# Kernel optimization log

Measured on AMD Instinct MI355X. Metric: run time of the kernel, lower is better.

The kernel has to match this reference:

```python
import jax, jax.numpy as jnp
import numpy as np

N_TOKENS = 16384
D_MODEL = 1024
N_SEG = 4
H_SEG = 1024  # intermediate_size (4096) // num_segments


def setup_inputs() -> dict:
    key = jax.random.key(0)
    kx, ki, kg, ku, kd = jax.random.split(key, 5)
    x = jax.random.normal(kx, (N_TOKENS, D_MODEL), dtype=jnp.float32)
    token_segment_indices = jax.random.randint(ki, (N_TOKENS,), 0, N_SEG, dtype=jnp.int64)
    s = 1.0 / np.sqrt(D_MODEL)
    # weights stored [seg, in, out] for x @ W
    gate_w = jax.random.normal(kg, (N_SEG, D_MODEL, H_SEG), dtype=jnp.float32) * s
    up_w = jax.random.normal(ku, (N_SEG, D_MODEL, H_SEG), dtype=jnp.float32) * s
    down_w = jax.random.normal(kd, (N_SEG, H_SEG, D_MODEL), dtype=jnp.float32) * (1.0 / np.sqrt(H_SEG))
    return {
        'x': x,
        'gate_w': gate_w,
        'up_w': up_w,
        'down_w': down_w,
        'token_segment_indices': token_segment_indices,
    }


def reference(x, gate_w, up_w, down_w, token_segment_indices):
    # _forward_with_indices: each token is processed only by its assigned
    # segment's SwiGLU FFN; all other contributions are zero.  We compute each
    # segment densely and mask (jit-friendly, same math as gather->ffn->scatter).
    out = jnp.zeros_like(x)
    for s in range(N_SEG):
        hidden = jax.nn.silu(x @ gate_w[s]) * (x @ up_w[s])  # [N, H_SEG]
        y = hidden @ down_w[s]                                # [N, D_MODEL]
        mask = (token_segment_indices == s)[:, None]
        out = out + jnp.where(mask, y, 0.0)
    return out
```

## Files before the change

### kernel.cpp

```cpp
#include <hip/hip_runtime.h>
#include <hip/hip_bf16.h>
#include <math.h>

#define NT   16384
#define DM   1024
#define NSEG 4
#define BK   64
#define HS   1024

typedef __attribute__((ext_vector_type(8))) short bf16x8;
typedef __attribute__((ext_vector_type(4))) float f32x4;

typedef __attribute__((address_space(1))) unsigned int gu32;
typedef __attribute__((address_space(3))) unsigned int lu32;

__device__ __forceinline__ void gll16(const void* g, void* l) {
  __builtin_amdgcn_global_load_lds((gu32*)(unsigned long long)g,
                                   (lu32*)(unsigned int)(unsigned long long)l,
                                   16, 0, 0);
}

__device__ __forceinline__ unsigned short cvt_bf16(float f) {
  unsigned int u = __float_as_uint(f);
  u += 0x7fffu + ((u >> 16) & 1u);
  return (unsigned short)(u >> 16);
}


__global__ __launch_bounds__(256) void k_prepw(
    const int* __restrict__ idx, int* __restrict__ part,
    const float* __restrict__ gw, const float* __restrict__ uw, const float* __restrict__ dw,
    unsigned short* __restrict__ gwt, unsigned short* __restrict__ uwt,
    unsigned short* __restrict__ dwt) {
  __shared__ float tile[64][65];
  const int bid = blockIdx.x, tid = threadIdx.x;
  if (bid < 64) {
    __shared__ int sc[5];
    if (tid < 5) sc[tid] = 0;
    __syncthreads();
    int lane = tid & 63;
    int w32 = idx[bid * 256 + tid];
    unsigned long long m = __ballot((tid & 1) && (w32 != 0));
    if (lane == 0 && m) atomicAdd(&sc[4], 1);
    __syncthreads();
    int is32 = (sc[4] != 0);
    int s = w32;
    if (!is32) s = idx[bid * 512 + 2 * tid];
#pragma unroll
    for (int q = 0; q < 4; ++q) {
      m = __ballot(s == q);
      if (lane == 0 && m) atomicAdd(&sc[q], (int)__popcll(m));
    }
    __syncthreads();
    if (tid < 4) part[bid * 8 + tid] = sc[tid];
    if (tid == 4) part[bid * 8 + 4] = is32;
    return;
  }
  int tb = bid - 64;
  int mtx = tb >> 10, seg = (tb >> 8) & 3, tl = tb & 255;
  const float* src = (mtx == 0 ? gw : mtx == 1 ? uw : dw) + (size_t)seg * DM * HS;
  unsigned short* dst = (mtx == 0 ? gwt : mtx == 1 ? uwt : dwt) + (size_t)seg * DM * HS;
  int n0 = (tl & 15) * 64, k0 = (tl >> 4) * 64;
  int col = tid & 63, rb = tid >> 6;
#pragma unroll
  for (int i = 0; i < 64; i += 4)
    tile[i + rb][col] = src[(size_t)(k0 + i + rb) * 1024 + n0 + col];
  __syncthreads();
  int kp = tid & 31, nb = tid >> 5;
#pragma unroll
  for (int j = 0; j < 64; j += 8) {
    int nn = j + nb;
    unsigned int w = (unsigned)cvt_bf16(tile[2 * kp][nn]) |
                     ((unsigned)cvt_bf16(tile[2 * kp + 1][nn]) << 16);
    *(unsigned int*)(dst + (size_t)(n0 + nn) * 1024 + k0 + 2 * kp) = w;
  }
}

__global__ __launch_bounds__(256) void k_cvtrank(
    const int* __restrict__ idx, const int* __restrict__ part,
    const float4* __restrict__ x,
    int* __restrict__ meta, int2* __restrict__ table,
    int* __restrict__ perm, uint4* __restrict__ xc) {
  __shared__ int cnt[64][4];
  __shared__ int wsum[4][4];
  __shared__ int tot[4], pref[4], gbase[4];
  __shared__ int rnk8[8];
  __shared__ int flag_s;
  const int tid = threadIdx.x, bid = blockIdx.x;
  const int lane = tid & 63, wv = tid >> 6;
  const int c = bid >> 5;
  const int p0 = (bid & 31) * 8;

  if (tid == 0) flag_s = part[c * 8 + 4];
  if (wv == 0) {
#pragma unroll
    for (int s = 0; s < 4; ++s) cnt[lane][s] = part[lane * 8 + s];
  }
  __syncthreads();
  const int is32 = flag_s;
  int tok = c * 256 + tid;
  int s_t = is32 ? idx[tok] : idx[2 * tok];
  int myr = 0;
  unsigned long long lt = (1ull << lane) - 1;
#pragma unroll
  for (int q = 0; q < 4; ++q) {
    unsigned long long m = __ballot(s_t == q);
    if (lane == 0) wsum[wv][q] = (int)__popcll(m);
    if (s_t == q) myr = (int)__popcll(m & lt);
  }
  __syncthreads();
  if (tid < 4) {
    int s = tid, t = 0, p = 0;
    for (int b = 0; b < 64; ++b) { if (b == c) p = t; t += cnt[b][s]; }
    tot[s] = t; pref[s] = p;
  }
  __syncthreads();
  if (tid == 0) {
    gbase[0] = 0;
    for (int s = 1; s < 4; ++s) gbase[s] = gbase[s - 1] + tot[s - 1];
    if (bid == 0) {
      int nt = 0;
      for (int s = 0; s < 4; ++s) {
        meta[s] = tot[s]; meta[5 + s] = gbase[s];
        for (int m0 = 0; m0 < tot[s]; m0 += 128) table[nt++] = make_int2(s, m0);
      }
      for (; nt < 132; ++nt) table[nt] = make_int2(-1, 0);
    }
  }
  __syncthreads();
  int wpre = 0;
  for (int w2 = 0; w2 < wv; ++w2) wpre += wsum[w2][s_t];
  int r = gbase[s_t] + pref[s_t] + wpre + myr;
  if (tid >= p0 && tid < p0 + 8) {
    perm[r] = tok;
    rnk8[tid - p0] = r;
  }
  __syncthreads();
  const int j = tid >> 5, l2 = tid & 31;
  const int tok8 = bid * 8 + j;
  const float4* src = x + (size_t)tok8 * 256;
  uint4* dst = xc + (size_t)rnk8[j] * 128;
#pragma unroll
  for (int it = 0; it < 4; ++it) {
    float4 a = src[it * 64 + l2 * 2];
    float4 b = src[it * 64 + l2 * 2 + 1];
    uint4 o;
    o.x = cvt_bf16(a.x) | ((unsigned)cvt_bf16(a.y) << 16);
    o.y = cvt_bf16(a.z) | ((unsigned)cvt_bf16(a.w) << 16);
    o.z = cvt_bf16(b.x) | ((unsigned)cvt_bf16(b.y) << 16);
    o.w = cvt_bf16(b.z) | ((unsigned)cvt_bf16(b.w) << 16);
    dst[it * 32 + l2] = o;
  }
}

__global__ __launch_bounds__(256) void k_gateup(
    const unsigned short* __restrict__ xc,
    const unsigned short* __restrict__ gwt,
    const unsigned short* __restrict__ uwt,
    const int* __restrict__ meta,
    const int2* __restrict__ table,
    unsigned short* __restrict__ hidden) {
  __shared__ __align__(16) unsigned short As[128 * BK];
  __shared__ __align__(16) unsigned short Bg[64 * BK];
  __shared__ __align__(16) unsigned short Bu[64 * BK];
  const int bid = blockIdx.x, tid = threadIdx.x;
  const int2 te = table[bid >> 4];
  if (te.x < 0) return;
  const int seg = te.x, m0 = te.y;
  const int count = meta[seg], base = meta[5 + seg];
  const int n0 = (bid & 15) * 64;

  const int lane = tid & 63;
  const int wave = tid >> 6;

  const unsigned short* ap[4];
#pragma unroll
  for (int is = 0; is < 4; ++is) {
    int c = is * 256 + tid;
    int m = c >> 3;
    int kb = (c & 7) ^ (m & 7);
    int row = m0 + m;
    row = row < count ? row : count - 1;
    ap[is] = xc + (size_t)(base + row) * DM + kb * 8;
  }
  const unsigned short *gp[2], *up[2];
#pragma unroll
  for (int is = 0; is < 2; ++is) {
    int c = is * 256 + tid;
    int n = c >> 3;
    int kb = (c & 7) ^ (n & 7);
    gp[is] = gwt + (size_t)(seg * HS + n0 + n) * DM + kb * 8;
    up[is] = uwt + (size_t)(seg * HS + n0 + n) * DM + kb * 8;
  }

  f32x4 accg[4][2] = {};
  f32x4 accu[4][2] = {};
  const int wm = (wave & 1) * 64;
  const int wn = (wave >> 1) * 32;
  const int fm = lane & 15;
  const int fq = lane >> 4;
  const int fx = lane & 7;
  const int a_e0 = (wm + fm) * 64 + ((fq) ^ fx) * 8;
  const int a_e1 = (wm + fm) * 64 + ((4 + fq) ^ fx) * 8;
  const int b_e0 = (wn + fm) * 64 + ((fq) ^ fx) * 8;
  const int b_e1 = (wn + fm) * 64 + ((4 + fq) ^ fx) * 8;

  for (int kt = 0; kt < DM / BK; ++kt) {
    __syncthreads();
#pragma unroll
    for (int is = 0; is < 4; ++is)
      gll16(ap[is], (char*)As + (is * 256 + wave * 64) * 16);
#pragma unroll
    for (int is = 0; is < 2; ++is) {
      gll16(gp[is], (char*)Bg + (is * 256 + wave * 64) * 16);
      gll16(up[is], (char*)Bu + (is * 256 + wave * 64) * 16);
    }
#pragma unroll
    for (int is = 0; is < 4; ++is) ap[is] += BK;
#pragma unroll
    for (int is = 0; is < 2; ++is) { gp[is] += BK; up[is] += BK; }
    __syncthreads();
#pragma unroll
    for (int s = 0; s < 2; ++s) {
      const unsigned short* Ap = As + (s ? a_e1 : a_e0);
      const unsigned short* Gp = Bg + (s ? b_e1 : b_e0);
      const unsigned short* Up = Bu + (s ? b_e1 : b_e0);
      bf16x8 af[4], bg2[2], bu2[2];
#pragma unroll
      for (int mi = 0; mi < 4; ++mi) af[mi] = *(const bf16x8*)(Ap + mi * 1024);
#pragma unroll
      for (int ni = 0; ni < 2; ++ni) {
        bg2[ni] = *(const bf16x8*)(Gp + ni * 1024);
        bu2[ni] = *(const bf16x8*)(Up + ni * 1024);
      }
#pragma unroll
      for (int mi = 0; mi < 4; ++mi)
#pragma unroll
        for (int ni = 0; ni < 2; ++ni) {
          accg[mi][ni] = __builtin_amdgcn_mfma_f32_16x16x32_bf16(af[mi], bg2[ni], accg[mi][ni], 0, 0, 0);
          accu[mi][ni] = __builtin_amdgcn_mfma_f32_16x16x32_bf16(af[mi], bu2[ni], accu[mi][ni], 0, 0, 0);
        }
    }
  }

  const int rq = fq * 4;
#pragma unroll
  for (int mi = 0; mi < 4; ++mi) {
#pragma unroll
    for (int r = 0; r < 4; ++r) {
      int row = m0 + wm + mi * 16 + rq + r;
      if (row < count) {
        unsigned short* h = hidden + (size_t)(base + row) * HS + n0 + wn;
#pragma unroll
        for (int ni = 0; ni < 2; ++ni) {
          float gv = accg[mi][ni][r];
          float uv = accu[mi][ni][r];
          float sig = 1.0f / (1.0f + __expf(-gv));
          h[ni * 16 + fm] = cvt_bf16(gv * sig * uv);
        }
      }
    }
  }
}

__global__ __launch_bounds__(256) void k_down(
    const unsigned short* __restrict__ hidden,
    const unsigned short* __restrict__ dwt,
    const int* __restrict__ meta,
    const int2* __restrict__ table,
    const int* __restrict__ perm,
    float* __restrict__ out) {
  __shared__ __align__(16) unsigned short As[128 * BK];
  __shared__ __align__(16) unsigned short Bs[128 * BK];
  const int bid = blockIdx.x, tid = threadIdx.x;
  const int2 te = table[bid >> 3];
  if (te.x < 0) return;
  const int seg = te.x, m0 = te.y;
  const int count = meta[seg], base = meta[5 + seg];
  const int n0 = (bid & 7) * 128;

  const int lane = tid & 63;
  const int wave = tid >> 6;

  const unsigned short *ap[4], *bp[4];
#pragma unroll
  for (int is = 0; is < 4; ++is) {
    int c = is * 256 + tid;
    int m = c >> 3;
    int kb = (c & 7) ^ (m & 7);
    int row = m0 + m;
    row = row < count ? row : count - 1;
    ap[is] = hidden + (size_t)(base + row) * HS + kb * 8;
    bp[is] = dwt + (size_t)(seg * DM + n0 + m) * HS + kb * 8;
  }

  f32x4 acc[4][4] = {};
  const int wm = (wave & 1) * 64;
  const int wn = (wave >> 1) * 64;
  const int fm = lane & 15;
  const int fq = lane >> 4;
  const int fx = lane & 7;
  const int a_e0 = (wm + fm) * 64 + ((fq) ^ fx) * 8;
  const int a_e1 = (wm + fm) * 64 + ((4 + fq) ^ fx) * 8;
  const int b_e0 = (wn + fm) * 64 + ((fq) ^ fx) * 8;
  const int b_e1 = (wn + fm) * 64 + ((4 + fq) ^ fx) * 8;

  for (int kt = 0; kt < HS / BK; ++kt) {
    __syncthreads();
#pragma unroll
    for (int is = 0; is < 4; ++is) {
      gll16(ap[is], (char*)As + (is * 256 + wave * 64) * 16);
      gll16(bp[is], (char*)Bs + (is * 256 + wave * 64) * 16);
    }
#pragma unroll
    for (int is = 0; is < 4; ++is) { ap[is] += BK; bp[is] += BK; }
    __syncthreads();
#pragma unroll
    for (int s = 0; s < 2; ++s) {
      const unsigned short* Ap = As + (s ? a_e1 : a_e0);
      const unsigned short* Bp = Bs + (s ? b_e1 : b_e0);
      bf16x8 af[4], bf[4];
#pragma unroll
      for (int mi = 0; mi < 4; ++mi) af[mi] = *(const bf16x8*)(Ap + mi * 1024);
#pragma unroll
      for (int ni = 0; ni < 4; ++ni) bf[ni] = *(const bf16x8*)(Bp + ni * 1024);
#pragma unroll
      for (int mi = 0; mi < 4; ++mi)
#pragma unroll
        for (int ni = 0; ni < 4; ++ni)
          acc[mi][ni] = __builtin_amdgcn_mfma_f32_16x16x32_bf16(af[mi], bf[ni], acc[mi][ni], 0, 0, 0);
    }
  }

  const int rq = fq * 4;
#pragma unroll
  for (int mi = 0; mi < 4; ++mi) {
#pragma unroll
    for (int r = 0; r < 4; ++r) {
      int row = m0 + wm + mi * 16 + rq + r;
      if (row < count) {
        int t = perm[base + row];
        float* o = out + (size_t)t * DM + n0 + wn;
#pragma unroll
        for (int ni = 0; ni < 4; ++ni)
          o[ni * 16 + fm] = acc[mi][ni][r];
      }
    }
  }
}


extern "C" void kernel_launch(void* const* d_in, const int* in_sizes, int n_in,
                              void* d_out, int out_size, void* d_ws, size_t ws_size,
                              hipStream_t stream) {
  const float* x  = (const float*)d_in[0];
  const float* gw = (const float*)d_in[1];
  const float* uw = (const float*)d_in[2];
  const float* dw = (const float*)d_in[3];
  const int* tsi  = (const int*)d_in[4];
  float* out = (float*)d_out;

  char* ws = (char*)d_ws;
  int*  meta  = (int*)ws;
  int*  part  = (int*)(ws + 256);
  int2* table = (int2*)(ws + 4096);
  int*  perm  = (int*)(ws + 8192);
  unsigned short* xc  = (unsigned short*)(ws + (1 << 18));
  unsigned short* gwt = xc + (size_t)NT * DM;
  unsigned short* uwt = gwt + (size_t)NSEG * HS * DM;
  unsigned short* dwt = uwt + (size_t)NSEG * HS * DM;
  unsigned short* hid = dwt + (size_t)NSEG * DM * HS;

  k_prepw<<<64 + 3072, 256, 0, stream>>>(tsi, part, gw, uw, dw, gwt, uwt, dwt);
  k_cvtrank<<<2048, 256, 0, stream>>>(tsi, part, (const float4*)x, meta, table, perm, (uint4*)xc);
  k_gateup<<<16 * 132, 256, 0, stream>>>(xc, gwt, uwt, meta, table, hid);
  k_down<<<8 * 132, 256, 0, stream>>>(hid, dwt, meta, table, perm, out);
}
```

Baseline: 316.2 us.

## Double-buffer LDS and enlarge M tiles to 256 with 512-thread blocks

Both GEMM kernels move to 256-row M tiles with 8 waves per block and double-buffered shared memory. Global-to-LDS loads for the next K step are interleaved with MFMA work on the current buffer, using explicit vmcnt waits and barriers instead of two full syncthreads per step. MFMA bursts are wrapped in s_setprio. This is meant to hide load latency and halve weight re-reads per token, at the cost of more LDS per block, fewer blocks in flight, and more padding waste on partial segment tiles.

```diff
diff --git a/kernel.cpp b/kernel.cpp
--- a/kernel.cpp
+++ b/kernel.cpp
@@ -7,6 +7,7 @@
 #define NSEG 4
 #define BK   64
 #define HS   1024
+#define TBLN 68
 
 typedef __attribute__((ext_vector_type(8))) short bf16x8;
 typedef __attribute__((ext_vector_type(4))) float f32x4;
@@ -25,7 +26,6 @@
   u += 0x7fffu + ((u >> 16) & 1u);
   return (unsigned short)(u >> 16);
 }
-
 
 __global__ __launch_bounds__(256) void k_prepw(
     const int* __restrict__ idx, int* __restrict__ part,
@@ -122,9 +122,9 @@
       int nt = 0;
       for (int s = 0; s < 4; ++s) {
         meta[s] = tot[s]; meta[5 + s] = gbase[s];
-        for (int m0 = 0; m0 < tot[s]; m0 += 128) table[nt++] = make_int2(s, m0);
+        for (int m0 = 0; m0 < tot[s]; m0 += 256) table[nt++] = make_int2(s, m0);
       }
-      for (; nt < 132; ++nt) table[nt] = make_int2(-1, 0);
+      for (; nt < TBLN; ++nt) table[nt] = make_int2(-1, 0);
     }
   }
   __syncthreads();
@@ -153,16 +153,37 @@
   }
 }
 
-__global__ __launch_bounds__(256) void k_gateup(
+#define WAITBAR(N) \
+  asm volatile("s_waitcnt vmcnt(" #N ") lgkmcnt(0)\n\ts_barrier" ::: "memory")
+
+#define LDF(BUF, CUR, RB, F)                                               \
+  F[0][0] = *(const bf16x8*)(&BUF[CUR][((RB) + fm) * 64] + x0);            \
+  F[0][1] = *(const bf16x8*)(&BUF[CUR][((RB) + fm) * 64] + x1);            \
+  F[1][0] = *(const bf16x8*)(&BUF[CUR][((RB) + 16 + fm) * 64] + x0);       \
+  F[1][1] = *(const bf16x8*)(&BUF[CUR][((RB) + 16 + fm) * 64] + x1);
+
+#define MM8(ACC, MH, NH, AF, BF)                                                                                            \
+  __builtin_amdgcn_s_setprio(1);                                                                                            \
+  ACC[2*(MH)+0][2*(NH)+0] = __builtin_amdgcn_mfma_f32_16x16x32_bf16(AF[0][0], BF[0][0], ACC[2*(MH)+0][2*(NH)+0], 0, 0, 0);  \
+  ACC[2*(MH)+0][2*(NH)+1] = __builtin_amdgcn_mfma_f32_16x16x32_bf16(AF[0][0], BF[1][0], ACC[2*(MH)+0][2*(NH)+1], 0, 0, 0);  \
+  ACC[2*(MH)+1][2*(NH)+0] = __builtin_amdgcn_mfma_f32_16x16x32_bf16(AF[1][0], BF[0][0], ACC[2*(MH)+1][2*(NH)+0], 0, 0, 0);  \
+  ACC[2*(MH)+1][2*(NH)+1] = __builtin_amdgcn_mfma_f32_16x16x32_bf16(AF[1][0], BF[1][0], ACC[2*(MH)+1][2*(NH)+1], 0, 0, 0);  \
+  ACC[2*(MH)+0][2*(NH)+0] = __builtin_amdgcn_mfma_f32_16x16x32_bf16(AF[0][1], BF[0][1], ACC[2*(MH)+0][2*(NH)+0], 0, 0, 0);  \
+  ACC[2*(MH)+0][2*(NH)+1] = __builtin_amdgcn_mfma_f32_16x16x32_bf16(AF[0][1], BF[1][1], ACC[2*(MH)+0][2*(NH)+1], 0, 0, 0);  \
+  ACC[2*(MH)+1][2*(NH)+0] = __builtin_amdgcn_mfma_f32_16x16x32_bf16(AF[1][1], BF[0][1], ACC[2*(MH)+1][2*(NH)+0], 0, 0, 0);  \
+  ACC[2*(MH)+1][2*(NH)+1] = __builtin_amdgcn_mfma_f32_16x16x32_bf16(AF[1][1], BF[1][1], ACC[2*(MH)+1][2*(NH)+1], 0, 0, 0);  \
+  __builtin_amdgcn_s_setprio(0);
+
+__global__ __launch_bounds__(512) void k_gateup(
     const unsigned short* __restrict__ xc,
     const unsigned short* __restrict__ gwt,
     const unsigned short* __restrict__ uwt,
     const int* __restrict__ meta,
     const int2* __restrict__ table,
     unsigned short* __restrict__ hidden) {
-  __shared__ __align__(16) unsigned short As[128 * BK];
-  __shared__ __align__(16) unsigned short Bg[64 * BK];
-  __shared__ __align__(16) unsigned short Bu[64 * BK];
+  __shared__ __align__(16) unsigned short As[2][256 * BK];
+  __shared__ __align__(16) unsigned short Bg[2][64 * BK];
+  __shared__ __align__(16) unsigned short Bu[2][64 * BK];
   const int bid = blockIdx.x, tid = threadIdx.x;
   const int2 te = table[bid >> 4];
   if (te.x < 0) return;
@@ -171,77 +192,84 @@
   const int n0 = (bid & 15) * 64;
 
   const int lane = tid & 63;
-  const int wave = tid >> 6;
-
-  const unsigned short* ap[4];
-#pragma unroll
-  for (int is = 0; is < 4; ++is) {
-    int c = is * 256 + tid;
-    int m = c >> 3;
-    int kb = (c & 7) ^ (m & 7);
-    int row = m0 + m;
-    row = row < count ? row : count - 1;
-    ap[is] = xc + (size_t)(base + row) * DM + kb * 8;
-  }
-  const unsigned short *gp[2], *up[2];
-#pragma unroll
-  for (int is = 0; is < 2; ++is) {
-    int c = is * 256 + tid;
-    int n = c >> 3;
-    int kb = (c & 7) ^ (n & 7);
-    gp[is] = gwt + (size_t)(seg * HS + n0 + n) * DM + kb * 8;
-    up[is] = uwt + (size_t)(seg * HS + n0 + n) * DM + kb * 8;
-  }
+  const int wv = tid >> 6;
+  const int l0 = lane >> 3, j = lane & 7;
+
+  const int rl0 = wv * 8, rl1 = 64 + wv * 8;
+  const int rb0 = (rl0 & 31) + (rl0 >> 5) * 64;
+  const int rb1 = (rl1 & 31) + (rl1 >> 5) * 64;
+  const int a0d0 = rb0 * 128, a0d1 = rb1 * 128;
+  const int a1d0 = a0d0 + 32 * 128, a1d1 = a0d1 + 32 * 128;
+  const int r00 = rb0 + l0, r01 = rb1 + l0;
+  const int r10 = r00 + 32, r11 = r01 + 32;
+  auto rowof = [&](int r) { int g = m0 + r; return g < count ? g : count - 1; };
+  const unsigned short* a0p0 = xc + (size_t)(base + rowof(r00)) * DM + (j ^ (r00 & 7)) * 8;
+  const unsigned short* a0p1 = xc + (size_t)(base + rowof(r01)) * DM + (j ^ (r01 & 7)) * 8;
+  const unsigned short* a1p0 = xc + (size_t)(base + rowof(r10)) * DM + (j ^ (r10 & 7)) * 8;
+  const unsigned short* a1p1 = xc + (size_t)(base + rowof(r11)) * DM + (j ^ (r11 & 7)) * 8;
+  const int nb = wv * 8 + l0;
+  const unsigned short* gp  = gwt + (size_t)(seg * HS + n0 + nb) * DM + (j ^ (nb & 7)) * 8;
+  const unsigned short* upp = uwt + (size_t)(seg * HS + n0 + nb) * DM + (j ^ (nb & 7)) * 8;
+  const int bd = wv * 1024;
+
+  const int wm = (wv & 3) * 64;
+  const int wn = (wv >> 2) * 32;
+  const int fm = lane & 15, fq = lane >> 4;
+  const int x0 = (fq ^ (fm & 7)) * 8;
+  const int x1 = ((4 + fq) ^ (fm & 7)) * 8;
 
   f32x4 accg[4][2] = {};
   f32x4 accu[4][2] = {};
-  const int wm = (wave & 1) * 64;
-  const int wn = (wave >> 1) * 32;
-  const int fm = lane & 15;
-  const int fq = lane >> 4;
-  const int fx = lane & 7;
-  const int a_e0 = (wm + fm) * 64 + ((fq) ^ fx) * 8;
-  const int a_e1 = (wm + fm) * 64 + ((4 + fq) ^ fx) * 8;
-  const int b_e0 = (wn + fm) * 64 + ((fq) ^ fx) * 8;
-  const int b_e1 = (wn + fm) * 64 + ((4 + fq) ^ fx) * 8;
-
-  for (int kt = 0; kt < DM / BK; ++kt) {
-    __syncthreads();
-#pragma unroll
-    for (int is = 0; is < 4; ++is)
-      gll16(ap[is], (char*)As + (is * 256 + wave * 64) * 16);
-#pragma unroll
-    for (int is = 0; is < 2; ++is) {
-      gll16(gp[is], (char*)Bg + (is * 256 + wave * 64) * 16);
-      gll16(up[is], (char*)Bu + (is * 256 + wave * 64) * 16);
-    }
-#pragma unroll
-    for (int is = 0; is < 4; ++is) ap[is] += BK;
-#pragma unroll
-    for (int is = 0; is < 2; ++is) { gp[is] += BK; up[is] += BK; }
-    __syncthreads();
-#pragma unroll
-    for (int s = 0; s < 2; ++s) {
-      const unsigned short* Ap = As + (s ? a_e1 : a_e0);
-      const unsigned short* Gp = Bg + (s ? b_e1 : b_e0);
-      const unsigned short* Up = Bu + (s ? b_e1 : b_e0);
-      bf16x8 af[4], bg2[2], bu2[2];
-#pragma unroll
-      for (int mi = 0; mi < 4; ++mi) af[mi] = *(const bf16x8*)(Ap + mi * 1024);
-#pragma unroll
-      for (int ni = 0; ni < 2; ++ni) {
-        bg2[ni] = *(const bf16x8*)(Gp + ni * 1024);
-        bu2[ni] = *(const bf16x8*)(Up + ni * 1024);
-      }
-#pragma unroll
-      for (int mi = 0; mi < 4; ++mi)
-#pragma unroll
-        for (int ni = 0; ni < 2; ++ni) {
-          accg[mi][ni] = __builtin_amdgcn_mfma_f32_16x16x32_bf16(af[mi], bg2[ni], accg[mi][ni], 0, 0, 0);
-          accu[mi][ni] = __builtin_amdgcn_mfma_f32_16x16x32_bf16(af[mi], bu2[ni], accu[mi][ni], 0, 0, 0);
-        }
-    }
-  }
+
+#define GU_ITER(CUR, NXT) {                                   \
+    bf16x8 af[2][2], af2[2][2], bg2[2][2], bu2[2][2];         \
+    gll16(a0p0, (char*)&As[NXT][0] + a0d0);                   \
+    gll16(a0p1, (char*)&As[NXT][0] + a0d1);                   \
+    WAITBAR(5);                                               \
+    LDF(As, CUR, wm, af); LDF(Bg, CUR, wn, bg2);              \
+    MM8(accg, 0, 0, af, bg2);                                 \
+    gll16(gp, (char*)&Bg[NXT][0] + bd);                       \
+    WAITBAR(5);                                               \
+    LDF(Bu, CUR, wn, bu2);                                    \
+    MM8(accu, 0, 0, af, bu2);                                 \
+    gll16(upp, (char*)&Bu[NXT][0] + bd);                      \
+    WAITBAR(4);                                               \
+    LDF(As, CUR, wm + 32, af2);                               \
+    MM8(accg, 1, 0, af2, bg2);                                \
+    gll16(a1p0, (char*)&As[NXT][0] + a1d0);                   \
+    gll16(a1p1, (char*)&As[NXT][0] + a1d1);                   \
+    MM8(accu, 1, 0, af2, bu2);                                \
+    a0p0 += BK; a0p1 += BK; a1p0 += BK; a1p1 += BK; gp += BK; upp += BK; \
+  }
+
+  gll16(a0p0, (char*)&As[0][0] + a0d0);
+  gll16(a0p1, (char*)&As[0][0] + a0d1);
+  gll16(gp,   (char*)&Bg[0][0] + bd);
+  gll16(upp,  (char*)&Bu[0][0] + bd);
+  gll16(a1p0, (char*)&As[0][0] + a1d0);
+  gll16(a1p1, (char*)&As[0][0] + a1d1);
+  a0p0 += BK; a0p1 += BK; a1p0 += BK; a1p1 += BK; gp += BK; upp += BK;
+
+#pragma unroll 1
+  for (int t7 = 0; t7 < 7; ++t7) {
+    GU_ITER(0, 1);
+    GU_ITER(1, 0);
+  }
+  GU_ITER(0, 1);
+  {
+    bf16x8 af[2][2], af2[2][2], bg2[2][2], bu2[2][2];
+    WAITBAR(3);
+    LDF(As, 1, wm, af); LDF(Bg, 1, wn, bg2);
+    MM8(accg, 0, 0, af, bg2);
+    WAITBAR(2);
+    LDF(Bu, 1, wn, bu2);
+    MM8(accu, 0, 0, af, bu2);
+    WAITBAR(0);
+    LDF(As, 1, wm + 32, af2);
+    MM8(accg, 1, 0, af2, bg2);
+    MM8(accu, 1, 0, af2, bu2);
+  }
+#undef GU_ITER
 
   const int rq = fq * 4;
 #pragma unroll
@@ -263,15 +291,15 @@
   }
 }
 
-__global__ __launch_bounds__(256) void k_down(
+__global__ __launch_bounds__(512) void k_down(
     const unsigned short* __restrict__ hidden,
     const unsigned short* __restrict__ dwt,
     const int* __restrict__ meta,
     const int2* __restrict__ table,
     const int* __restrict__ perm,
     float* __restrict__ out) {
-  __shared__ __align__(16) unsigned short As[128 * BK];
-  __shared__ __align__(16) unsigned short Bs[128 * BK];
+  __shared__ __align__(16) unsigned short As[2][256 * BK];
+  __shared__ __align__(16) unsigned short Bs[2][128 * BK];
   const int bid = blockIdx.x, tid = threadIdx.x;
   const int2 te = table[bid >> 3];
   if (te.x < 0) return;
@@ -280,57 +308,87 @@
   const int n0 = (bid & 7) * 128;
 
   const int lane = tid & 63;
-  const int wave = tid >> 6;
-
-  const unsigned short *ap[4], *bp[4];
-#pragma unroll
-  for (int is = 0; is < 4; ++is) {
-    int c = is * 256 + tid;
-    int m = c >> 3;
-    int kb = (c & 7) ^ (m & 7);
-    int row = m0 + m;
-    row = row < count ? row : count - 1;
-    ap[is] = hidden + (size_t)(base + row) * HS + kb * 8;
-    bp[is] = dwt + (size_t)(seg * DM + n0 + m) * HS + kb * 8;
-  }
+  const int wv = tid >> 6;
+  const int l0 = lane >> 3, j = lane & 7;
+
+  const int rl0 = wv * 8, rl1 = 64 + wv * 8;
+  const int rb0 = (rl0 & 31) + (rl0 >> 5) * 64;
+  const int rb1 = (rl1 & 31) + (rl1 >> 5) * 64;
+  const int a0d0 = rb0 * 128, a0d1 = rb1 * 128;
+  const int a1d0 = a0d0 + 32 * 128, a1d1 = a0d1 + 32 * 128;
+  const int r00 = rb0 + l0, r01 = rb1 + l0;
+  const int r10 = r00 + 32, r11 = r01 + 32;
+  auto rowof = [&](int r) { int g = m0 + r; return g < count ? g : count - 1; };
+  const unsigned short* a0p0 = hidden + (size_t)(base + rowof(r00)) * HS + (j ^ (r00 & 7)) * 8;
+  const unsigned short* a0p1 = hidden + (size_t)(base + rowof(r01)) * HS + (j ^ (r01 & 7)) * 8;
+  const unsigned short* a1p0 = hidden + (size_t)(base + rowof(r10)) * HS + (j ^ (r10 & 7)) * 8;
+  const unsigned short* a1p1 = hidden + (size_t)(base + rowof(r11)) * HS + (j ^ (r11 & 7)) * 8;
+  const int nl = wv * 8 + l0;
+  const int nb0 = (nl & 31) + (nl >> 5) * 64;
+  const int nb1 = nb0 + 32;
+  const unsigned short* bp0 = dwt + (size_t)(seg * DM + n0 + nb0) * HS + (j ^ (nb0 & 7)) * 8;
+  const unsigned short* bp1 = dwt + (size_t)(seg * DM + n0 + nb1) * HS + (j ^ (nb1 & 7)) * 8;
+  const int bw = wv * 8;
+  const int bd0 = ((bw & 31) + (bw >> 5) * 64) * 128;
+  const int bd1 = bd0 + 32 * 128;
+
+  const int wm = (wv & 3) * 64;
+  const int wn = (wv >> 2) * 64;
+  const int fm = lane & 15, fq = lane >> 4;
+  const int x0 = (fq ^ (fm & 7)) * 8;
+  const int x1 = ((4 + fq) ^ (fm & 7)) * 8;
 
   f32x4 acc[4][4] = {};
-  const int wm = (wave & 1) * 64;
-  const int wn = (wave >> 1) * 64;
-  const int fm = lane & 15;
-  const int fq = lane >> 4;
-  const int fx = lane & 7;
-  const int a_e0 = (wm + fm) * 64 + ((fq) ^ fx) * 8;
-  const int a_e1 = (wm + fm) * 64 + ((4 + fq) ^ fx) * 8;
-  const int b_e0 = (wn + fm) * 64 + ((fq) ^ fx) * 8;
-  const int b_e1 = (wn + fm) * 64 + ((4 + fq) ^ fx) * 8;
-
-  for (int kt = 0; kt < HS / BK; ++kt) {
-    __syncthreads();
-#pragma unroll
-    for (int is = 0; is < 4; ++is) {
-      gll16(ap[is], (char*)As + (is * 256 + wave * 64) * 16);
-      gll16(bp[is], (char*)Bs + (is * 256 + wave * 64) * 16);
-    }
-#pragma unroll
-    for (int is = 0; is < 4; ++is) { ap[is] += BK; bp[is] += BK; }
-    __syncthreads();
-#pragma unroll
-    for (int s = 0; s < 2; ++s) {
-      const unsigned short* Ap = As + (s ? a_e1 : a_e0);
-      const unsigned short* Bp = Bs + (s ? b_e1 : b_e0);
-      bf16x8 af[4], bf[4];
-#pragma unroll
-      for (int mi = 0; mi < 4; ++mi) af[mi] = *(const bf16x8*)(Ap + mi * 1024);
-#pragma unroll
-      for (int ni = 0; ni < 4; ++ni) bf[ni] = *(const bf16x8*)(Bp + ni * 1024);
-#pragma unroll
-      for (int mi = 0; mi < 4; ++mi)
-#pragma unroll
-        for (int ni = 0; ni < 4; ++ni)
-          acc[mi][ni] = __builtin_amdgcn_mfma_f32_16x16x32_bf16(af[mi], bf[ni], acc[mi][ni], 0, 0, 0);
-    }
-  }
+
+#define DN_ITER(CUR, NXT) {                                   \
+    bf16x8 af[2][2], af2[2][2], b0[2][2], b1[2][2];           \
+    gll16(a0p0, (char*)&As[NXT][0] + a0d0);                   \
+    gll16(a0p1, (char*)&As[NXT][0] + a0d1);                   \
+    WAITBAR(5);                                               \
+    LDF(As, CUR, wm, af); LDF(Bs, CUR, wn, b0);               \
+    MM8(acc, 0, 0, af, b0);                                   \
+    gll16(bp0, (char*)&Bs[NXT][0] + bd0);                     \
+    WAITBAR(5);                                               \
+    LDF(Bs, CUR, wn + 32, b1);                                \
+    MM8(acc, 0, 1, af, b1);                                   \
+    gll16(bp1, (char*)&Bs[NXT][0] + bd1);                     \
+    WAITBAR(4);                                               \
+    LDF(As, CUR, wm + 32, af2);                               \
+    MM8(acc, 1, 0, af2, b0);                                  \
+    gll16(a1p0, (char*)&As[NXT][0] + a1d0);                   \
+    gll16(a1p1, (char*)&As[NXT][0] + a1d1);                   \
+    MM8(acc, 1, 1, af2, b1);                                  \
+    a0p0 += BK; a0p1 += BK; a1p0 += BK; a1p1 += BK; bp0 += BK; bp1 += BK; \
+  }
+
+  gll16(a0p0, (char*)&As[0][0] + a0d0);
+  gll16(a0p1, (char*)&As[0][0] + a0d1);
+  gll16(bp0,  (char*)&Bs[0][0] + bd0);
+  gll16(bp1,  (char*)&Bs[0][0] + bd1);
+  gll16(a1p0, (char*)&As[0][0] + a1d0);
+  gll16(a1p1, (char*)&As[0][0] + a1d1);
+  a0p0 += BK; a0p1 += BK; a1p0 += BK; a1p1 += BK; bp0 += BK; bp1 += BK;
+
+#pragma unroll 1
+  for (int t7 = 0; t7 < 7; ++t7) {
+    DN_ITER(0, 1);
+    DN_ITER(1, 0);
+  }
+  DN_ITER(0, 1);
+  {
+    bf16x8 af[2][2], af2[2][2], b0[2][2], b1[2][2];
+    WAITBAR(3);
+    LDF(As, 1, wm, af); LDF(Bs, 1, wn, b0);
+    MM8(acc, 0, 0, af, b0);
+    WAITBAR(2);
+    LDF(Bs, 1, wn + 32, b1);
+    MM8(acc, 0, 1, af, b1);
+    WAITBAR(0);
+    LDF(As, 1, wm + 32, af2);
+    MM8(acc, 1, 0, af2, b0);
+    MM8(acc, 1, 1, af2, b1);
+  }
+#undef DN_ITER
 
   const int rq = fq * 4;
 #pragma unroll
@@ -373,6 +431,6 @@
 
   k_prepw<<<64 + 3072, 256, 0, stream>>>(tsi, part, gw, uw, dw, gwt, uwt, dwt);
   k_cvtrank<<<2048, 256, 0, stream>>>(tsi, part, (const float4*)x, meta, table, perm, (uint4*)xc);
-  k_gateup<<<16 * 132, 256, 0, stream>>>(xc, gwt, uwt, meta, table, hid);
-  k_down<<<8 * 132, 256, 0, stream>>>(hid, dwt, meta, table, perm, out);
-}
+  k_gateup<<<16 * TBLN, 512, 0, stream>>>(xc, gwt, uwt, meta, table, hid);
+  k_down<<<8 * TBLN, 512, 0, stream>>>(hid, dwt, meta, table, perm, out);
+}
```

Result: faster. 307.8 us (-2.7%).
